# Optimization experiments

Measured on AMD Instinct MI355X. Metric: run time of the kernel, lower is better.

Reference implementation:

```python
import jax, jax.numpy as jnp
import numpy as np

NUM_EXPERTS = 8
TOP_K = 2
D_IN = 1024
D_OUT = 1024
N_TOKENS = 8192


def setup_inputs() -> dict:
    key = jax.random.key(0)
    ks = jax.random.split(key, 7)
    s_in = 1.0 / np.sqrt(D_IN)
    s_out = 1.0 / np.sqrt(D_OUT)
    return {
        "x": jax.random.normal(ks[0], (N_TOKENS, D_IN), dtype=jnp.float32),
        # stacked expert params: fc1 [E, D_in, D_out], fc2 [E, D_out, D_out]
        "W1": jax.random.uniform(ks[1], (NUM_EXPERTS, D_IN, D_OUT), jnp.float32, -s_in, s_in),
        "b1": jax.random.uniform(ks[2], (NUM_EXPERTS, D_OUT), jnp.float32, -s_in, s_in),
        "W2": jax.random.uniform(ks[3], (NUM_EXPERTS, D_OUT, D_OUT), jnp.float32, -s_out, s_out),
        "b2": jax.random.uniform(ks[4], (NUM_EXPERTS, D_OUT), jnp.float32, -s_out, s_out),
        "Wg": jax.random.uniform(ks[5], (D_IN, NUM_EXPERTS), jnp.float32, -s_in, s_in),
        "bg": jax.random.uniform(ks[6], (NUM_EXPERTS,), jnp.float32, -s_in, s_in),
    }


def reference(x, W1, b1, W2, b2, Wg, bg):
    n = x.shape[0]
    # gating
    gate_logits = x @ Wg + bg                      # [N, E]
    gate_weights = jax.nn.softmax(gate_logits, axis=1)
    if TOP_K < NUM_EXPERTS:
        topk_vals, topk_idx = jax.lax.top_k(gate_weights, TOP_K)  # [N, K]
        rows = jnp.arange(n)[:, None]
        gate_weights = jnp.zeros_like(gate_weights).at[rows, topk_idx].set(topk_vals)
    # dense all-expert MLP fan-out (faithful to the original wasteful compute)
    h = jax.nn.relu(jnp.einsum('nd,edh->enh', x, W1) + b1[:, None, :])  # [E, N, H]
    y = jnp.einsum('enh,eho->eno', h, W2) + b2[:, None, :]               # [E, N, O]
    # weighted combine over experts
    out = jnp.einsum('ne,eno->no', gate_weights, y)                      # [N, O]
    return out
```

## Files before the change

kernel.cpp:

```cpp
#include <hip/hip_runtime.h>

#define NUM_E 8
#define N_TOK 8192
#define DIM 1024

typedef __attribute__((ext_vector_type(8))) short short8;
typedef __attribute__((ext_vector_type(4))) float f32x4;

__device__ __forceinline__ unsigned short f2bf(float f) {
  unsigned int u = __float_as_uint(f);
  u = (u + 0x7fffu + ((u >> 16) & 1u)) >> 16;
  return (unsigned short)u;
}

__device__ __forceinline__ void async16(const unsigned short* g, unsigned short* l) {
  __builtin_amdgcn_global_load_lds((const __attribute__((address_space(1))) void*)g,
                                   (__attribute__((address_space(3))) void*)l,
                                   16, 0, 0);
}


__global__ __launch_bounds__(256) void convert_x_kernel(const float* __restrict__ x,
                                                        unsigned short* __restrict__ xb) {
  size_t i = ((size_t)blockIdx.x * 256 + threadIdx.x) * 8;
  float4 v0 = *(const float4*)(x + i);
  float4 v1 = *(const float4*)(x + i + 4);
  union { unsigned short u[8]; uint4 v; } o;
  o.u[0] = f2bf(v0.x); o.u[1] = f2bf(v0.y); o.u[2] = f2bf(v0.z); o.u[3] = f2bf(v0.w);
  o.u[4] = f2bf(v1.x); o.u[5] = f2bf(v1.y); o.u[6] = f2bf(v1.z); o.u[7] = f2bf(v1.w);
  *(uint4*)(xb + i) = o.v;
}

__global__ __launch_bounds__(256) void convert_w_kernel(const float* __restrict__ W1,
                                                        const float* __restrict__ W2,
                                                        unsigned short* __restrict__ W1T,
                                                        unsigned short* __restrict__ W2T) {
  int tid = blockIdx.x * 256 + threadIdx.x;
  int n   = tid & 1023;
  int kc  = (tid >> 10) & 127;
  int mat = tid >> 17;
  const float* src;
  unsigned short* dst;
  if (mat < 8) { src = W1 + (size_t)mat * (DIM * DIM); dst = W1T + (size_t)mat * (DIM * DIM); }
  else         { src = W2 + (size_t)(mat - 8) * (DIM * DIM); dst = W2T + (size_t)(mat - 8) * (DIM * DIM); }
  const int k0 = kc * 8;
  union { unsigned short u[8]; uint4 v; } o;
#pragma unroll
  for (int j = 0; j < 8; ++j)
    o.u[j] = f2bf(src[(size_t)(k0 + j) * DIM + n]);
  *(uint4*)(dst + (size_t)n * DIM + k0) = o.v;
}

__global__ __launch_bounds__(256) void gate1_kernel(const float* __restrict__ x,
                                                    const float* __restrict__ Wg,
                                                    const float* __restrict__ bg,
                                                    int* __restrict__ tok_top,
                                                    float2* __restrict__ tok_wts) {
  const int wave = threadIdx.x >> 6;
  const int lane = threadIdx.x & 63;
  const int n = blockIdx.x * 4 + wave;
  const float4* xr = (const float4*)(x + (size_t)n * DIM);
  float acc[NUM_E];
#pragma unroll
  for (int e = 0; e < NUM_E; ++e) acc[e] = 0.f;
#pragma unroll
  for (int it = 0; it < 4; ++it) {
    float4 xv = xr[it * 64 + lane];
    const float4* wr = (const float4*)Wg + (size_t)(it * 256 + lane * 4) * 2;
    float xs[4] = {xv.x, xv.y, xv.z, xv.w};
#pragma unroll
    for (int dd = 0; dd < 4; ++dd) {
      float4 wa = wr[dd * 2 + 0];
      float4 wb = wr[dd * 2 + 1];
      acc[0] += xs[dd] * wa.x; acc[1] += xs[dd] * wa.y;
      acc[2] += xs[dd] * wa.z; acc[3] += xs[dd] * wa.w;
      acc[4] += xs[dd] * wb.x; acc[5] += xs[dd] * wb.y;
      acc[6] += xs[dd] * wb.z; acc[7] += xs[dd] * wb.w;
    }
  }
#pragma unroll
  for (int e = 0; e < NUM_E; ++e)
#pragma unroll
    for (int off = 32; off > 0; off >>= 1)
      acc[e] += __shfl_down(acc[e], off);
  if (lane == 0) {
    float p[NUM_E];
    float mx = -1e30f;
#pragma unroll
    for (int e = 0; e < NUM_E; ++e) { p[e] = acc[e] + bg[e]; mx = fmaxf(mx, p[e]); }
    float s = 0.f;
#pragma unroll
    for (int e = 0; e < NUM_E; ++e) { p[e] = expf(p[e] - mx); s += p[e]; }
    float inv = 1.f / s;
    int i0 = 0;
#pragma unroll
    for (int e = 1; e < NUM_E; ++e) if (p[e] > p[i0]) i0 = e;
    int i1 = (i0 == 0) ? 1 : 0;
#pragma unroll
    for (int e = 0; e < NUM_E; ++e) if (e != i0 && p[e] > p[i1]) i1 = e;
    tok_top[n] = i0 | (i1 << 8);
    tok_wts[n] = make_float2(p[i0] * inv, p[i1] * inv);
  }
}

__global__ __launch_bounds__(1024) void gate2_kernel(const int* __restrict__ tok_top,
                                                     const float2* __restrict__ tok_wts,
                                                     int* __restrict__ counts,
                                                     int* __restrict__ tok_idx,
                                                     float* __restrict__ tok_w) {
  const int e = blockIdx.x;
  const int t = threadIdx.x;
  const int lane = t & 63;
  const int wave = t >> 6;
  __shared__ int wsum[16];
  __shared__ int blocktot;
  int match[8];
  float w[8];
  int cnt = 0;
#pragma unroll
  for (int j = 0; j < 8; ++j) {
    int n = t * 8 + j;
    int top = tok_top[n];
    float2 ww = tok_wts[n];
    bool m0 = (top & 0xff) == e;
    bool m1 = ((top >> 8) & 0xff) == e;
    match[j] = (m0 || m1) ? 1 : 0;
    w[j] = m0 ? ww.x : ww.y;
    cnt += match[j];
  }
  int inc = cnt;
#pragma unroll
  for (int off = 1; off < 64; off <<= 1) {
    int v = __shfl_up(inc, off);
    if (lane >= off) inc += v;
  }
  if (lane == 63) wsum[wave] = inc;
  __syncthreads();
  if (t < 16) {
    int v = wsum[t];
    int s = v;
#pragma unroll
    for (int off = 1; off < 16; off <<= 1) {
      int u = __shfl_up(s, off);
      if (lane >= off) s += u;
    }
    wsum[t] = s - v;
    if (t == 15) blocktot = s;
  }
  __syncthreads();
  int slot = wsum[wave] + inc - cnt;
#pragma unroll
  for (int j = 0; j < 8; ++j) {
    if (match[j]) {
      tok_idx[e * N_TOK + slot] = t * 8 + j;
      tok_w[e * N_TOK + slot] = w[j];
      slot++;
    }
  }
  if (t == 0) counts[e] = blocktot;
}


template <bool FC1>
__global__ __launch_bounds__(256, 2) void moe_gemm_kernel(
    const unsigned short* __restrict__ A_src,
    const unsigned short* __restrict__ wT,
    const float* __restrict__ bias,
    const int* __restrict__ counts,
    const int* __restrict__ tok_idx,
    const float* __restrict__ tok_w,
    unsigned short* __restrict__ h_out,
    float* __restrict__ out)
{
  const int e = blockIdx.z;
  const int count = counts[e];
  const int m0 = blockIdx.y * 128;
  if (m0 >= count) return;
  const int n0 = blockIdx.x * 128;

  int base = 0;
#pragma unroll
  for (int i = 0; i < NUM_E; ++i) base += (i < e) ? ((counts[i] + 127) & ~127) : 0;

  const int tid  = threadIdx.x;
  const int wave = tid >> 6;
  const int lane = tid & 63;
  const int l15  = lane & 15;
  const int quad = lane >> 4;
  const int wm   = wave & 1;
  const int wn   = wave >> 1;

  __shared__ unsigned short sA[128 * 32];
  __shared__ unsigned short sB[128 * 32];
  __shared__ int   s_tok[128];
  __shared__ float s_w[128];

  if (!FC1 && tid < 128) {
    int slot = m0 + tid;
    int cs = slot < count ? slot : count - 1;
    s_tok[tid] = tok_idx[e * N_TOK + cs];
    s_w[tid]   = slot < count ? tok_w[e * N_TOK + slot] : 0.f;
  }

  const int r0 = 32 * wave + l15;
  const int r1 = r0 + 16;
  size_t aOff0, aOff1;
  if (FC1) {
    int s0 = m0 + r0; s0 = s0 < count ? s0 : count - 1;
    int s1 = m0 + r1; s1 = s1 < count ? s1 : count - 1;
    aOff0 = (size_t)tok_idx[e * N_TOK + s0] * DIM;
    aOff1 = (size_t)tok_idx[e * N_TOK + s1] * DIM;
  } else {
    aOff0 = (size_t)(base + m0 + r0) * DIM;
    aOff1 = (size_t)(base + m0 + r1) * DIM;
  }
  const unsigned short* wte = wT + (size_t)e * DIM * DIM;
  const size_t bOff0 = (size_t)(n0 + r0) * DIM;
  const size_t bOff1 = (size_t)(n0 + r1) * DIM;
  const int kl = quad * 8;

  unsigned short* ldsA0 = &sA[(2 * wave + 0) * 512];
  unsigned short* ldsA1 = &sA[(2 * wave + 1) * 512];
  unsigned short* ldsB0 = &sB[(2 * wave + 0) * 512];
  unsigned short* ldsB1 = &sB[(2 * wave + 1) * 512];

  const f32x4 vzero = {0.f, 0.f, 0.f, 0.f};
  f32x4 acc[4][4];
#pragma unroll
  for (int i = 0; i < 4; ++i)
#pragma unroll
    for (int j = 0; j < 4; ++j) acc[i][j] = vzero;

  for (int k0 = 0; k0 < DIM; k0 += 32) {
    async16(A_src + aOff0 + k0 + kl, ldsA0);
    async16(A_src + aOff1 + k0 + kl, ldsA1);
    async16(wte + bOff0 + k0 + kl, ldsB0);
    async16(wte + bOff1 + k0 + kl, ldsB1);
    asm volatile("s_waitcnt vmcnt(0)" ::: "memory");
    __syncthreads();
    short8 af[4], bfr[4];
#pragma unroll
    for (int i = 0; i < 4; ++i)
      af[i] = *(const short8*)&sA[(wm * 4 + i) * 512 + lane * 8];
#pragma unroll
    for (int j = 0; j < 4; ++j)
      bfr[j] = *(const short8*)&sB[(wn * 4 + j) * 512 + lane * 8];
#pragma unroll
    for (int i = 0; i < 4; ++i)
#pragma unroll
      for (int j = 0; j < 4; ++j)
        acc[i][j] = __builtin_amdgcn_mfma_f32_16x16x32_bf16(af[i], bfr[j], acc[i][j], 0, 0, 0);
    __syncthreads();
  }

  float bv[4];
#pragma unroll
  for (int j = 0; j < 4; ++j)
    bv[j] = bias[e * DIM + n0 + (wn * 4 + j) * 16 + l15];

  if (FC1) {
#pragma unroll
    for (int i = 0; i < 4; ++i) {
      const int rbase = (wm * 4 + i) * 16 + quad * 4;
#pragma unroll
      for (int r = 0; r < 4; ++r) {
        const int slot = m0 + rbase + r;
        if (slot < count) {
          unsigned short* hp = h_out + (size_t)(base + slot) * DIM + n0;
#pragma unroll
          for (int j = 0; j < 4; ++j) {
            float v = acc[i][j][r] + bv[j];
            v = v > 0.f ? v : 0.f;
            hp[(wn * 4 + j) * 16 + l15] = f2bf(v);
          }
        }
      }
    }
  } else {
#pragma unroll
    for (int i = 0; i < 4; ++i) {
      const int rbase = (wm * 4 + i) * 16 + quad * 4;
#pragma unroll
      for (int r = 0; r < 4; ++r) {
        const int slot = m0 + rbase + r;
        if (slot < count) {
          const int rl = rbase + r;
          const int tok = s_tok[rl];
          const float w = s_w[rl];
          float* op = out + (size_t)tok * DIM + n0;
#pragma unroll
          for (int j = 0; j < 4; ++j) {
            float v = acc[i][j][r] + bv[j];
            atomicAdd(&op[(wn * 4 + j) * 16 + l15], w * v);
          }
        }
      }
    }
  }
}


extern "C" void kernel_launch(void* const* d_in, const int* in_sizes, int n_in,
                              void* d_out, int out_size, void* d_ws, size_t ws_size,
                              hipStream_t stream) {
  const float* x  = (const float*)d_in[0];
  const float* W1 = (const float*)d_in[1];
  const float* b1 = (const float*)d_in[2];
  const float* W2 = (const float*)d_in[3];
  const float* b2 = (const float*)d_in[4];
  const float* Wg = (const float*)d_in[5];
  const float* bg = (const float*)d_in[6];
  float* out = (float*)d_out;

  char* ws = (char*)d_ws;
  int*            counts  = (int*)(ws);
  int*            tok_idx = (int*)(ws + 1024);
  float*          tok_w   = (float*)(ws + 263168);
  unsigned short* xb      = (unsigned short*)(ws + 525312);
  unsigned short* w1t     = (unsigned short*)(ws + 525312 + 16777216ull);
  unsigned short* w2t     = (unsigned short*)(ws + 525312 + 2ull * 16777216ull);
  unsigned short* hb      = (unsigned short*)(ws + 525312 + 3ull * 16777216ull);
  size_t gate_off = 525312 + 3ull * 16777216ull + 35651584ull;
  int*            tok_top = (int*)(ws + gate_off);
  float2*         tok_wts = (float2*)(ws + gate_off + 32768);

  hipMemsetAsync(d_out, 0, (size_t)N_TOK * DIM * sizeof(float), stream);

  convert_x_kernel<<<N_TOK * DIM / (8 * 256), 256, 0, stream>>>(x, xb);
  convert_w_kernel<<<2 * NUM_E * DIM * (DIM / 8) / 256, 256, 0, stream>>>(W1, W2, w1t, w2t);
  gate1_kernel<<<N_TOK / 4, 256, 0, stream>>>(x, Wg, bg, tok_top, tok_wts);
  gate2_kernel<<<NUM_E, 1024, 0, stream>>>(tok_top, tok_wts, counts, tok_idx, tok_w);
  moe_gemm_kernel<true><<<dim3(8, 64, NUM_E), 256, 0, stream>>>(
      xb, w1t, b1, counts, tok_idx, tok_w, hb, nullptr);
  moe_gemm_kernel<false><<<dim3(8, 64, NUM_E), 256, 0, stream>>>(
      hb, w2t, b2, counts, tok_idx, tok_w, nullptr, out);
}
```

Before: 425.7 us.

## Triple-buffer GEMM K loop, fuse x conversion into gating, reorder grid

The MoE GEMM main loop moves from a single LDS buffer with a full wait and two barriers per K step to a three-stage ring of async global-to-LDS loads. The loop waits only for the current stage and keeps two stages in flight, so global load latency overlaps with MFMA work. The bf16 conversion of x is folded into the gating kernel, which already reads x, removing one kernel and one full pass over x. The grid is reordered so the expert index is the fastest block dimension, and launch bounds are raised to three blocks per CU. The cost is triple the LDS footprint and more register pressure under the tighter occupancy bound.

```diff
diff --git a/kernel.cpp b/kernel.cpp
--- a/kernel.cpp
+++ b/kernel.cpp
@@ -17,18 +17,6 @@
   __builtin_amdgcn_global_load_lds((const __attribute__((address_space(1))) void*)g,
                                    (__attribute__((address_space(3))) void*)l,
                                    16, 0, 0);
-}
-
-
-__global__ __launch_bounds__(256) void convert_x_kernel(const float* __restrict__ x,
-                                                        unsigned short* __restrict__ xb) {
-  size_t i = ((size_t)blockIdx.x * 256 + threadIdx.x) * 8;
-  float4 v0 = *(const float4*)(x + i);
-  float4 v1 = *(const float4*)(x + i + 4);
-  union { unsigned short u[8]; uint4 v; } o;
-  o.u[0] = f2bf(v0.x); o.u[1] = f2bf(v0.y); o.u[2] = f2bf(v0.z); o.u[3] = f2bf(v0.w);
-  o.u[4] = f2bf(v1.x); o.u[5] = f2bf(v1.y); o.u[6] = f2bf(v1.z); o.u[7] = f2bf(v1.w);
-  *(uint4*)(xb + i) = o.v;
 }
 
 __global__ __launch_bounds__(256) void convert_w_kernel(const float* __restrict__ W1,
@@ -55,11 +43,13 @@
                                                     const float* __restrict__ Wg,
                                                     const float* __restrict__ bg,
                                                     int* __restrict__ tok_top,
-                                                    float2* __restrict__ tok_wts) {
+                                                    float2* __restrict__ tok_wts,
+                                                    unsigned short* __restrict__ xb) {
   const int wave = threadIdx.x >> 6;
   const int lane = threadIdx.x & 63;
   const int n = blockIdx.x * 4 + wave;
   const float4* xr = (const float4*)(x + (size_t)n * DIM);
+  unsigned short* xbr = xb + (size_t)n * DIM;
   float acc[NUM_E];
 #pragma unroll
   for (int e = 0; e < NUM_E; ++e) acc[e] = 0.f;
@@ -68,6 +58,10 @@
     float4 xv = xr[it * 64 + lane];
     const float4* wr = (const float4*)Wg + (size_t)(it * 256 + lane * 4) * 2;
     float xs[4] = {xv.x, xv.y, xv.z, xv.w};
+    union { unsigned short u[4]; uint2 v; } oo;
+    oo.u[0] = f2bf(xv.x); oo.u[1] = f2bf(xv.y);
+    oo.u[2] = f2bf(xv.z); oo.u[3] = f2bf(xv.w);
+    *(uint2*)(xbr + it * 256 + lane * 4) = oo.v;
 #pragma unroll
     for (int dd = 0; dd < 4; ++dd) {
       float4 wa = wr[dd * 2 + 0];
@@ -162,7 +156,7 @@
 
 
 template <bool FC1>
-__global__ __launch_bounds__(256, 2) void moe_gemm_kernel(
+__global__ __launch_bounds__(256, 3) void moe_gemm_kernel(
     const unsigned short* __restrict__ A_src,
     const unsigned short* __restrict__ wT,
     const float* __restrict__ bias,
@@ -172,11 +166,11 @@
     unsigned short* __restrict__ h_out,
     float* __restrict__ out)
 {
-  const int e = blockIdx.z;
+  const int e = blockIdx.x;
   const int count = counts[e];
-  const int m0 = blockIdx.y * 128;
+  const int m0 = blockIdx.z * 128;
   if (m0 >= count) return;
-  const int n0 = blockIdx.x * 128;
+  const int n0 = blockIdx.y * 128;
 
   int base = 0;
 #pragma unroll
@@ -190,16 +184,19 @@
   const int wm   = wave & 1;
   const int wn   = wave >> 1;
 
-  __shared__ unsigned short sA[128 * 32];
-  __shared__ unsigned short sB[128 * 32];
+  __shared__ unsigned short sA[3][128 * 32];
+  __shared__ unsigned short sB[3][128 * 32];
   __shared__ int   s_tok[128];
   __shared__ float s_w[128];
 
-  if (!FC1 && tid < 128) {
-    int slot = m0 + tid;
-    int cs = slot < count ? slot : count - 1;
-    s_tok[tid] = tok_idx[e * N_TOK + cs];
-    s_w[tid]   = slot < count ? tok_w[e * N_TOK + slot] : 0.f;
+  if (!FC1) {
+    if (tid < 128) {
+      int slot = m0 + tid;
+      int cs = slot < count ? slot : count - 1;
+      s_tok[tid] = tok_idx[e * N_TOK + cs];
+      s_w[tid]   = slot < count ? tok_w[e * N_TOK + slot] : 0.f;
+    }
+    __syncthreads();
   }
 
   const int r0 = 32 * wave + l15;
@@ -218,11 +215,8 @@
   const size_t bOff0 = (size_t)(n0 + r0) * DIM;
   const size_t bOff1 = (size_t)(n0 + r1) * DIM;
   const int kl = quad * 8;
-
-  unsigned short* ldsA0 = &sA[(2 * wave + 0) * 512];
-  unsigned short* ldsA1 = &sA[(2 * wave + 1) * 512];
-  unsigned short* ldsB0 = &sB[(2 * wave + 0) * 512];
-  unsigned short* ldsB1 = &sB[(2 * wave + 1) * 512];
+  const int c0 = (2 * wave + 0) * 512;
+  const int c1 = (2 * wave + 1) * 512;
 
   const f32x4 vzero = {0.f, 0.f, 0.f, 0.f};
   f32x4 acc[4][4];
@@ -231,26 +225,37 @@
 #pragma unroll
     for (int j = 0; j < 4; ++j) acc[i][j] = vzero;
 
-  for (int k0 = 0; k0 < DIM; k0 += 32) {
-    async16(A_src + aOff0 + k0 + kl, ldsA0);
-    async16(A_src + aOff1 + k0 + kl, ldsA1);
-    async16(wte + bOff0 + k0 + kl, ldsB0);
-    async16(wte + bOff1 + k0 + kl, ldsB1);
-    asm volatile("s_waitcnt vmcnt(0)" ::: "memory");
-    __syncthreads();
+  auto stage = [&](int kt, int b) {
+    const int koff = kt * 32 + kl;
+    async16(A_src + aOff0 + koff, &sA[b][c0]);
+    async16(A_src + aOff1 + koff, &sA[b][c1]);
+    async16(wte + bOff0 + koff, &sB[b][c0]);
+    async16(wte + bOff1 + koff, &sB[b][c1]);
+  };
+
+  stage(0, 0);
+  stage(1, 1);
+#pragma unroll
+  for (int kt = 0; kt < 32; ++kt) {
+    const int cur = kt % 3;
+    if (kt + 1 < 32) {
+      asm volatile("s_waitcnt vmcnt(4)\n\ts_barrier" ::: "memory");
+    } else {
+      asm volatile("s_waitcnt vmcnt(0)\n\ts_barrier" ::: "memory");
+    }
+    if (kt + 2 < 32) stage(kt + 2, (kt + 2) % 3);
     short8 af[4], bfr[4];
 #pragma unroll
     for (int i = 0; i < 4; ++i)
-      af[i] = *(const short8*)&sA[(wm * 4 + i) * 512 + lane * 8];
+      af[i] = *(const short8*)&sA[cur][(wm * 4 + i) * 512 + lane * 8];
 #pragma unroll
     for (int j = 0; j < 4; ++j)
-      bfr[j] = *(const short8*)&sB[(wn * 4 + j) * 512 + lane * 8];
+      bfr[j] = *(const short8*)&sB[cur][(wn * 4 + j) * 512 + lane * 8];
 #pragma unroll
     for (int i = 0; i < 4; ++i)
 #pragma unroll
       for (int j = 0; j < 4; ++j)
         acc[i][j] = __builtin_amdgcn_mfma_f32_16x16x32_bf16(af[i], bfr[j], acc[i][j], 0, 0, 0);
-    __syncthreads();
   }
 
   float bv[4];
@@ -326,12 +331,11 @@
 
   hipMemsetAsync(d_out, 0, (size_t)N_TOK * DIM * sizeof(float), stream);
 
-  convert_x_kernel<<<N_TOK * DIM / (8 * 256), 256, 0, stream>>>(x, xb);
   convert_w_kernel<<<2 * NUM_E * DIM * (DIM / 8) / 256, 256, 0, stream>>>(W1, W2, w1t, w2t);
-  gate1_kernel<<<N_TOK / 4, 256, 0, stream>>>(x, Wg, bg, tok_top, tok_wts);
+  gate1_kernel<<<N_TOK / 4, 256, 0, stream>>>(x, Wg, bg, tok_top, tok_wts, xb);
   gate2_kernel<<<NUM_E, 1024, 0, stream>>>(tok_top, tok_wts, counts, tok_idx, tok_w);
-  moe_gemm_kernel<true><<<dim3(8, 64, NUM_E), 256, 0, stream>>>(
+  moe_gemm_kernel<true><<<dim3(NUM_E, 8, 64), 256, 0, stream>>>(
       xb, w1t, b1, counts, tok_idx, tok_w, hb, nullptr);
-  moe_gemm_kernel<false><<<dim3(8, 64, NUM_E), 256, 0, stream>>>(
+  moe_gemm_kernel<false><<<dim3(NUM_E, 8, 64), 256, 0, stream>>>(
       hb, w2t, b2, counts, tok_idx, tok_w, nullptr, out);
 }
```

Result: faster. 398.8 us (-6.3%).
